# Performance work log

Measured on AMD Instinct MI355X. Metric: run time of the kernel, lower is better.

Reference implementation:

```python
import jax, jax.numpy as jnp
import numpy as np

N, E = 10000, 320000
NF, HF = 256, 256  # input_nf/output_nf, hidden_nf
EPS = 1e-8


def setup_inputs() -> dict:
    key = jax.random.key(0)
    ks = jax.random.split(key, 20)
    h = jax.random.normal(ks[0], (N, NF), jnp.float32)
    coord = jax.random.normal(ks[1], (N, 3), jnp.float32)
    edge_index = jax.random.randint(ks[2], (2, E), 0, N, jnp.int32)

    def dense(k, fan_in, fan_out, scale=None):
        s = scale if scale is not None else 1.0 / np.sqrt(fan_in)
        W = jax.random.normal(k, (fan_in, fan_out), jnp.float32) * s
        b = jnp.zeros((fan_out,), jnp.float32)
        return W, b

    We1, be1 = dense(ks[3], 2 * NF + 1, HF)   # edge_mlp layer 1
    We2, be2 = dense(ks[4], HF, HF)           # edge_mlp layer 2
    Wn1, bn1 = dense(ks[5], HF + NF, HF)      # node_mlp layer 1
    Wn2, bn2 = dense(ks[6], HF, NF)           # node_mlp layer 2
    Wc1, bc1 = dense(ks[7], HF, HF)           # coord_mlp layer 1
    Wc2, bc2 = dense(ks[8], HF, 1, scale=0.001)  # coord_mlp final, tiny init (xavier gain=0.001)
    return dict(h=h, coord=coord, edge_index=edge_index,
                We1=We1, be1=be1, We2=We2, be2=be2,
                Wn1=Wn1, bn1=bn1, Wn2=Wn2, bn2=bn2,
                Wc1=Wc1, bc1=bc1, Wc2=Wc2, bc2=bc2)


def _segment_sum(data, seg_ids, num_segments):
    return jax.ops.segment_sum(data, seg_ids, num_segments=num_segments)


def reference(h, coord, edge_index, We1, be1, We2, be2, Wn1, bn1, Wn2, bn2, Wc1, bc1, Wc2, bc2):
    row, col = edge_index[0], edge_index[1]

    # coord2radial
    coord_diff = coord[row] - coord[col]                    # [E, 3]
    radial = jnp.sum(coord_diff ** 2, axis=1, keepdims=True)  # [E, 1]

    # edge model: MLP on [h_i, h_j, ||x_i - x_j||^2]
    edge_in = jnp.concatenate([h[row], h[col], radial], axis=1)  # [E, 2*NF+1]
    e = jax.nn.silu(edge_in @ We1 + be1)
    edge_feat = jax.nn.silu(e @ We2 + be2)                  # [E, HF]

    # coord model: coord_diff * coord_mlp(edge_feat), mean-aggregated
    c = jax.nn.silu(edge_feat @ Wc1 + bc1)
    trans = coord_diff * (c @ Wc2 + bc2)                    # [E, 3]
    agg_c = _segment_sum(trans, row, coord.shape[0])
    count = _segment_sum(jnp.ones_like(trans), row, coord.shape[0])
    coord_out = coord + agg_c / jnp.clip(count, 1.0)

    # node model: sum-aggregate edge features, concat with h, MLP
    agg_h = _segment_sum(edge_feat, row, h.shape[0])        # [N, HF]
    node_in = jnp.concatenate([h, agg_h], axis=1)           # [N, HF+NF]
    n = jax.nn.silu(node_in @ Wn1 + bn1)
    h_out = n @ Wn2 + bn2                                   # [N, NF]

    return h_out, coord_out
```

## Files before the change

kernel.cpp:

```cpp
#include <hip/hip_runtime.h>
#include <hip/hip_bf16.h>

typedef __bf16 bf16;
typedef __attribute__((ext_vector_type(8))) __bf16 bf16x8;
typedef __attribute__((ext_vector_type(4))) float f32x4;

static_assert(sizeof(bf16x8) == 16, "bf16x8 must be 16B");

constexpr int N_NODES = 10000;
constexpr int N_EDGES = 320000;
constexpr int KPAD    = 264;

__device__ __forceinline__ float silu_f(float x) { return x / (1.0f + __expf(-x)); }

__device__ __forceinline__ unsigned pk_bf16(float lo, float hi) {
  unsigned a = __float_as_uint(lo) + 0x8000u;
  unsigned b = __float_as_uint(hi) + 0x8000u;
  return __builtin_amdgcn_perm(b, a, 0x07060302u);
}

__device__ __forceinline__ void mfmaT_k256(const bf16* __restrict__ WT, int wstride, int koff,
                                           const bf16* Albs, int w, int r, int q, f32x4 acc[4][4]) {
  for (int k0 = 0; k0 < 256; k0 += 32) {
    bf16x8 a[4], b[4];
#pragma unroll
    for (int mi = 0; mi < 4; ++mi)
      a[mi] = *(const bf16x8*)(WT + (size_t)(w * 64 + 16 * mi + r) * wstride + koff + k0 + q * 8);
#pragma unroll
    for (int ni = 0; ni < 4; ++ni)
      b[ni] = *(const bf16x8*)(Albs + (16 * ni + r) * KPAD + k0 + q * 8);
#pragma unroll
    for (int mi = 0; mi < 4; ++mi)
#pragma unroll
      for (int ni = 0; ni < 4; ++ni)
        acc[mi][ni] = __builtin_amdgcn_mfma_f32_16x16x32_bf16(a[mi], b[ni], acc[mi][ni], 0, 0, 0);
  }
}

__global__ __launch_bounds__(256) void prep_kernel(
    const float* __restrict__ h, const float* __restrict__ We1, const float* __restrict__ We2,
    const float* __restrict__ Wn1, const float* __restrict__ Wn2, const float* __restrict__ Wc1,
    const int* __restrict__ eidx,
    bf16* __restrict__ Hb, bf16* __restrict__ We1T, bf16* __restrict__ Wn1T,
    bf16* __restrict__ We2T, bf16* __restrict__ Wn2T, bf16* __restrict__ Wc1T,
    int* __restrict__ hist) {
  int bid = blockIdx.x, tid = threadIdx.x;
  if (bid < 10000) { int i = bid * 256 + tid; Hb[i] = (bf16)h[i]; return; }
  if (bid >= 11792) {
    int e = (bid - 11792) * 256 + tid;
    if (e < N_EDGES) atomicAdd(&hist[eidx[e]], 1);
    return;
  }
  int t = (bid - 10000) * 256 + tid;
  if (t < 131072) { int k = t >> 8, j = t & 255; We1T[j * 512 + k] = (bf16)We1[k * 256 + j]; return; }
  t -= 131072;
  if (t < 131072) { int k = t >> 8, j = t & 255; Wn1T[j * 512 + k] = (bf16)Wn1[k * 256 + j]; return; }
  t -= 131072;
  if (t < 65536) { int k = t >> 8, j = t & 255; We2T[j * 256 + k] = (bf16)We2[k * 256 + j]; return; }
  t -= 65536;
  if (t < 65536) { int k = t >> 8, j = t & 255; Wn2T[j * 256 + k] = (bf16)Wn2[k * 256 + j]; return; }
  t -= 65536;
  if (t < 65536) { int k = t >> 8, j = t & 255; Wc1T[j * 256 + k] = (bf16)Wc1[k * 256 + j]; return; }
}

__global__ __launch_bounds__(256) void scan_kernel(const int* __restrict__ hist,
                                                   int* __restrict__ base, int* __restrict__ cursor) {
  __shared__ int partial[256];
  int t = threadIdx.x;
  int s = 0;
  for (int i = 0; i < 40; ++i) { int idx = t * 40 + i; if (idx < N_NODES) s += hist[idx]; }
  partial[t] = s;
  __syncthreads();
  for (int d = 1; d < 256; d <<= 1) {
    int v = (t >= d) ? partial[t - d] : 0;
    __syncthreads();
    partial[t] += v;
    __syncthreads();
  }
  int run = partial[t] - s;
  for (int i = 0; i < 40; ++i) {
    int idx = t * 40 + i;
    if (idx < N_NODES) { base[idx] = run; cursor[idx] = run; run += hist[idx]; }
  }
}

__global__ __launch_bounds__(256) void scatter_kernel(const int* __restrict__ eidx, int* __restrict__ cursor,
                                                      int* __restrict__ rs, int* __restrict__ cs) {
  int e = blockIdx.x * 256 + threadIdx.x;
  if (e < N_EDGES) {
    int r = eidx[e], c = eidx[N_EDGES + e];
    int p = atomicAdd(&cursor[r], 1);
    rs[p] = r; cs[p] = c;
  }
}

__global__ __launch_bounds__(256, 2) void gemm_pq(const bf16* __restrict__ Hb,
                                                  const bf16* __restrict__ We1T,
                                                  const float* __restrict__ be1,
                                                  bf16* __restrict__ P, bf16* __restrict__ Q) {
  int tid = threadIdx.x, w = tid >> 6, lane = tid & 63, r = lane & 15, q = lane >> 4;
  int m0 = blockIdx.x * 64;
  int koff = blockIdx.y ? 256 : 0;
  bf16* OUT = blockIdx.y ? Q : P;
  bool addb = (blockIdx.y == 0);
  f32x4 acc[4][4];
#pragma unroll
  for (int mi = 0; mi < 4; ++mi)
#pragma unroll
    for (int ni = 0; ni < 4; ++ni) acc[mi][ni] = (f32x4){0.f, 0.f, 0.f, 0.f};

  for (int k0 = 0; k0 < 256; k0 += 32) {
    bf16x8 a[4], b[4];
#pragma unroll
    for (int mi = 0; mi < 4; ++mi)
      a[mi] = *(const bf16x8*)(We1T + (size_t)(w * 64 + 16 * mi + r) * 512 + koff + k0 + q * 8);
#pragma unroll
    for (int ni = 0; ni < 4; ++ni) {
      int m = m0 + 16 * ni + r; if (m > N_NODES - 1) m = N_NODES - 1;
      b[ni] = *(const bf16x8*)(Hb + (size_t)m * 256 + k0 + q * 8);
    }
#pragma unroll
    for (int mi = 0; mi < 4; ++mi)
#pragma unroll
      for (int ni = 0; ni < 4; ++ni)
        acc[mi][ni] = __builtin_amdgcn_mfma_f32_16x16x32_bf16(a[mi], b[ni], acc[mi][ni], 0, 0, 0);
  }
#pragma unroll
  for (int mi = 0; mi < 4; ++mi) {
    int ch = w * 64 + 16 * mi + 4 * q;
    float4 bv = addb ? *(const float4*)(be1 + ch) : (float4){0.f, 0.f, 0.f, 0.f};
#pragma unroll
    for (int ni = 0; ni < 4; ++ni) {
      int m = m0 + 16 * ni + r;
      if (m < N_NODES) {
        uint2 o;
        o.x = pk_bf16(acc[mi][ni][0] + bv.x, acc[mi][ni][1] + bv.y);
        o.y = pk_bf16(acc[mi][ni][2] + bv.z, acc[mi][ni][3] + bv.w);
        *(uint2*)(OUT + (size_t)m * 256 + ch) = o;
      }
    }
  }
}

__global__ __launch_bounds__(256, 4) void edge_kernel(
    const float* __restrict__ coord, const int* __restrict__ rs, const int* __restrict__ cs,
    const float* __restrict__ We1,
    const float* __restrict__ be2, const float* __restrict__ bc1,
    const float* __restrict__ Wc2, const float* __restrict__ bc2,
    const bf16* __restrict__ P, const bf16* __restrict__ Q,
    const bf16* __restrict__ We2T, const bf16* __restrict__ Wc1T,
    float* __restrict__ agg_h, float* __restrict__ agg_c) {
  __shared__ __align__(16) bf16 buf[64 * KPAD];
  __shared__ int s_row[64], s_col[64];
  __shared__ float s_rad[64], s_cd[64][3], s_part[64][4], s_scal[64];
  __shared__ int s_rs[65];
  __shared__ int s_nrun;

  int tid = threadIdx.x;
  int e0 = blockIdx.x * 64;
  int w = tid >> 6, lane = tid & 63, r = lane & 15, q = lane >> 4;

  if (tid < 64) {
    int e = e0 + tid;
    int ri = rs[e], ci = cs[e];
    s_row[tid] = ri; s_col[tid] = ci;
    float dx = coord[3 * ri + 0] - coord[3 * ci + 0];
    float dy = coord[3 * ri + 1] - coord[3 * ci + 1];
    float dz = coord[3 * ri + 2] - coord[3 * ci + 2];
    s_cd[tid][0] = dx; s_cd[tid][1] = dy; s_cd[tid][2] = dz;
    s_rad[tid] = dx * dx + dy * dy + dz * dz;
  }
  __syncthreads();

  if (tid < 64) {
    bool bnd = (tid == 0) || (s_row[tid] != s_row[tid - 1]);
    unsigned long long m = __ballot(bnd);
    int rank = __popcll(m & ((1ull << tid) - 1ull));
    if (bnd) s_rs[rank] = tid;
    if (tid == 0) { int R = __popcll(m); s_nrun = R; s_rs[R] = 64; }
  }

  {
    int off = (tid & 31) * 8;
    int esub = tid >> 5;
    float4 wa = *(const float4*)(We1 + 512 * 256 + off);
    float4 wb = *(const float4*)(We1 + 512 * 256 + off + 4);
#pragma unroll
    for (int p = 0; p < 8; ++p) {
      int e = p * 8 + esub;
      int ri = s_row[e], ci = s_col[e];
      bf16x8 pv = *(const bf16x8*)(P + (size_t)ri * 256 + off);
      bf16x8 qv = *(const bf16x8*)(Q + (size_t)ci * 256 + off);
      float rad = s_rad[e];
      float f0 = silu_f((float)pv[0] + (float)qv[0] + rad * wa.x);
      float f1 = silu_f((float)pv[1] + (float)qv[1] + rad * wa.y);
      float f2 = silu_f((float)pv[2] + (float)qv[2] + rad * wa.z);
      float f3 = silu_f((float)pv[3] + (float)qv[3] + rad * wa.w);
      float f4 = silu_f((float)pv[4] + (float)qv[4] + rad * wb.x);
      float f5 = silu_f((float)pv[5] + (float)qv[5] + rad * wb.y);
      float f6 = silu_f((float)pv[6] + (float)qv[6] + rad * wb.z);
      float f7 = silu_f((float)pv[7] + (float)qv[7] + rad * wb.w);
      uint4 o;
      o.x = pk_bf16(f0, f1); o.y = pk_bf16(f2, f3);
      o.z = pk_bf16(f4, f5); o.w = pk_bf16(f6, f7);
      *(uint4*)(buf + e * KPAD + off) = o;
    }
  }
  __syncthreads();

  {
    f32x4 acc[4][4];
#pragma unroll
    for (int mi = 0; mi < 4; ++mi)
#pragma unroll
      for (int ni = 0; ni < 4; ++ni) acc[mi][ni] = (f32x4){0.f, 0.f, 0.f, 0.f};
    mfmaT_k256(We2T, 256, 0, buf, w, r, q, acc);
    __syncthreads();
#pragma unroll
    for (int mi = 0; mi < 4; ++mi) {
      int ch = w * 64 + 16 * mi + 4 * q;
      float4 bv = *(const float4*)(be2 + ch);
#pragma unroll
      for (int ni = 0; ni < 4; ++ni) {
        int edge = 16 * ni + r;
        float f0 = silu_f(acc[mi][ni][0] + bv.x);
        float f1 = silu_f(acc[mi][ni][1] + bv.y);
        float f2 = silu_f(acc[mi][ni][2] + bv.z);
        float f3 = silu_f(acc[mi][ni][3] + bv.w);
        uint2 o; o.x = pk_bf16(f0, f1); o.y = pk_bf16(f2, f3);
        *(uint2*)(buf + edge * KPAD + ch) = o;
      }
    }
  }
  __syncthreads();

  f32x4 acc2[4][4];
#pragma unroll
  for (int mi = 0; mi < 4; ++mi)
#pragma unroll
    for (int ni = 0; ni < 4; ++ni) acc2[mi][ni] = (f32x4){0.f, 0.f, 0.f, 0.f};
  mfmaT_k256(Wc1T, 256, 0, buf, w, r, q, acc2);

  {
    int R = s_nrun;
    for (int rr = 0; rr < R; ++rr) {
      int st = s_rs[rr], en = s_rs[rr + 1];
      float s = 0.f;
      for (int e = st; e < en; ++e) s += (float)buf[e * KPAD + tid];
      atomicAdd(&agg_h[(size_t)s_row[st] * 256 + tid], s);
    }
  }
  __syncthreads();

#pragma unroll
  for (int mi = 0; mi < 4; ++mi) {
    int ch = w * 64 + 16 * mi + 4 * q;
    float4 bv = *(const float4*)(bc1 + ch);
#pragma unroll
    for (int ni = 0; ni < 4; ++ni) {
      int edge = 16 * ni + r;
      float f0 = silu_f(acc2[mi][ni][0] + bv.x);
      float f1 = silu_f(acc2[mi][ni][1] + bv.y);
      float f2 = silu_f(acc2[mi][ni][2] + bv.z);
      float f3 = silu_f(acc2[mi][ni][3] + bv.w);
      uint2 o; o.x = pk_bf16(f0, f1); o.y = pk_bf16(f2, f3);
      *(uint2*)(buf + edge * KPAD + ch) = o;
    }
  }
  __syncthreads();

  {
    int e = tid >> 2, p = tid & 3;
    float s = 0.f;
#pragma unroll
    for (int kk = 0; kk < 64; kk += 8) {
      bf16x8 v = *(const bf16x8*)(buf + e * KPAD + p * 64 + kk);
      float4 w0 = *(const float4*)(Wc2 + p * 64 + kk);
      float4 w1 = *(const float4*)(Wc2 + p * 64 + kk + 4);
      s += (float)v[0] * w0.x + (float)v[1] * w0.y + (float)v[2] * w0.z + (float)v[3] * w0.w
         + (float)v[4] * w1.x + (float)v[5] * w1.y + (float)v[6] * w1.z + (float)v[7] * w1.w;
    }
    s_part[e][p] = s;
  }
  __syncthreads();
  if (tid < 64)
    s_scal[tid] = s_part[tid][0] + s_part[tid][1] + s_part[tid][2] + s_part[tid][3] + bc2[0];
  __syncthreads();

  if (tid < 3) {
    int R = s_nrun;
    for (int rr = 0; rr < R; ++rr) {
      int st = s_rs[rr], en = s_rs[rr + 1];
      float s = 0.f;
      for (int e = st; e < en; ++e) s += s_cd[e][tid] * s_scal[e];
      atomicAdd(&agg_c[3 * s_row[st] + tid], s);
    }
  }
}

__global__ __launch_bounds__(256, 2) void node_kernel(
    const bf16* __restrict__ Hb, const float* __restrict__ agg_h,
    const int* __restrict__ hist, const float* __restrict__ coord, const float* __restrict__ agg_c,
    const bf16* __restrict__ Wn1T, const bf16* __restrict__ Wn2T,
    const float* __restrict__ bn1, const float* __restrict__ bn2,
    float* __restrict__ h_out, float* __restrict__ coord_out) {
  __shared__ __align__(16) bf16 buf[64 * KPAD];
  int tid = threadIdx.x, w = tid >> 6, lane = tid & 63, r = lane & 15, q = lane >> 4;
  int m0 = blockIdx.x * 64;

  if (tid < 64) {
    int m = m0 + tid;
    if (m < N_NODES) {
      float c = (float)hist[m]; if (c < 1.f) c = 1.f;
      coord_out[3 * m + 0] = coord[3 * m + 0] + agg_c[3 * m + 0] / c;
      coord_out[3 * m + 1] = coord[3 * m + 1] + agg_c[3 * m + 1] / c;
      coord_out[3 * m + 2] = coord[3 * m + 2] + agg_c[3 * m + 2] / c;
    }
  }

  f32x4 acc[4][4];
#pragma unroll
  for (int mi = 0; mi < 4; ++mi)
#pragma unroll
    for (int ni = 0; ni < 4; ++ni) acc[mi][ni] = (f32x4){0.f, 0.f, 0.f, 0.f};
  for (int k0 = 0; k0 < 256; k0 += 32) {
    bf16x8 a[4], b[4];
#pragma unroll
    for (int mi = 0; mi < 4; ++mi)
      a[mi] = *(const bf16x8*)(Wn1T + (size_t)(w * 64 + 16 * mi + r) * 512 + k0 + q * 8);
#pragma unroll
    for (int ni = 0; ni < 4; ++ni) {
      int m = m0 + 16 * ni + r; if (m > N_NODES - 1) m = N_NODES - 1;
      b[ni] = *(const bf16x8*)(Hb + (size_t)m * 256 + k0 + q * 8);
    }
#pragma unroll
    for (int mi = 0; mi < 4; ++mi)
#pragma unroll
      for (int ni = 0; ni < 4; ++ni)
        acc[mi][ni] = __builtin_amdgcn_mfma_f32_16x16x32_bf16(a[mi], b[ni], acc[mi][ni], 0, 0, 0);
  }
  for (int k0 = 0; k0 < 256; k0 += 32) {
    bf16x8 a[4], b[4];
#pragma unroll
    for (int mi = 0; mi < 4; ++mi)
      a[mi] = *(const bf16x8*)(Wn1T + (size_t)(w * 64 + 16 * mi + r) * 512 + 256 + k0 + q * 8);
#pragma unroll
    for (int ni = 0; ni < 4; ++ni) {
      int m = m0 + 16 * ni + r; if (m > N_NODES - 1) m = N_NODES - 1;
      const float* ap = agg_h + (size_t)m * 256 + k0 + q * 8;
      float4 u = *(const float4*)ap;
      float4 v = *(const float4*)(ap + 4);
      uint4 o;
      o.x = pk_bf16(u.x, u.y); o.y = pk_bf16(u.z, u.w);
      o.z = pk_bf16(v.x, v.y); o.w = pk_bf16(v.z, v.w);
      b[ni] = *(const bf16x8*)&o;
    }
#pragma unroll
    for (int mi = 0; mi < 4; ++mi)
#pragma unroll
      for (int ni = 0; ni < 4; ++ni)
        acc[mi][ni] = __builtin_amdgcn_mfma_f32_16x16x32_bf16(a[mi], b[ni], acc[mi][ni], 0, 0, 0);
  }
  __syncthreads();
#pragma unroll
  for (int mi = 0; mi < 4; ++mi) {
    int ch = w * 64 + 16 * mi + 4 * q;
    float4 bv = *(const float4*)(bn1 + ch);
#pragma unroll
    for (int ni = 0; ni < 4; ++ni) {
      int lm = 16 * ni + r;
      float f0 = silu_f(acc[mi][ni][0] + bv.x);
      float f1 = silu_f(acc[mi][ni][1] + bv.y);
      float f2 = silu_f(acc[mi][ni][2] + bv.z);
      float f3 = silu_f(acc[mi][ni][3] + bv.w);
      uint2 o; o.x = pk_bf16(f0, f1); o.y = pk_bf16(f2, f3);
      *(uint2*)(buf + lm * KPAD + ch) = o;
    }
  }
  __syncthreads();
  f32x4 acc2[4][4];
#pragma unroll
  for (int mi = 0; mi < 4; ++mi)
#pragma unroll
    for (int ni = 0; ni < 4; ++ni) acc2[mi][ni] = (f32x4){0.f, 0.f, 0.f, 0.f};
  mfmaT_k256(Wn2T, 256, 0, buf, w, r, q, acc2);
#pragma unroll
  for (int mi = 0; mi < 4; ++mi) {
    int ch = w * 64 + 16 * mi + 4 * q;
    float4 bv = *(const float4*)(bn2 + ch);
#pragma unroll
    for (int ni = 0; ni < 4; ++ni) {
      int m = m0 + 16 * ni + r;
      if (m < N_NODES) {
        float4 o;
        o.x = acc2[mi][ni][0] + bv.x;
        o.y = acc2[mi][ni][1] + bv.y;
        o.z = acc2[mi][ni][2] + bv.z;
        o.w = acc2[mi][ni][3] + bv.w;
        *(float4*)(h_out + (size_t)m * 256 + ch) = o;
      }
    }
  }
}

extern "C" void kernel_launch(void* const* d_in, const int* in_sizes, int n_in,
                              void* d_out, int out_size, void* d_ws, size_t ws_size,
                              hipStream_t stream) {
  const float* h     = (const float*)d_in[0];
  const float* coord = (const float*)d_in[1];
  const int*   eidx  = (const int*)d_in[2];
  const float* We1 = (const float*)d_in[3];
  const float* be1 = (const float*)d_in[4];
  const float* We2 = (const float*)d_in[5];
  const float* be2 = (const float*)d_in[6];
  const float* Wn1 = (const float*)d_in[7];
  const float* bn1 = (const float*)d_in[8];
  const float* Wn2 = (const float*)d_in[9];
  const float* bn2 = (const float*)d_in[10];
  const float* Wc1 = (const float*)d_in[11];
  const float* bc1 = (const float*)d_in[12];
  const float* Wc2 = (const float*)d_in[13];
  const float* bc2 = (const float*)d_in[14];

  char* ws = (char*)d_ws;
  float* agg_h = (float*)(ws + 0);
  float* agg_c = (float*)(ws + 10240000);
  int*   hist  = (int*)  (ws + 10360000);
  int*   base  = (int*)  (ws + 10400000);
  int*   cursor= (int*)  (ws + 10440000);
  int*   rs    = (int*)  (ws + 10480000);
  int*   cs    = (int*)  (ws + 11760000);
  bf16* Hb   = (bf16*)(ws + 13040000);
  bf16* P    = (bf16*)(ws + 18160000);
  bf16* Q    = (bf16*)(ws + 23280000);
  bf16* We1T = (bf16*)(ws + 28400000);
  bf16* Wn1T = (bf16*)(ws + 28662144);
  bf16* We2T = (bf16*)(ws + 28924288);
  bf16* Wn2T = (bf16*)(ws + 29055360);
  bf16* Wc1T = (bf16*)(ws + 29186432);

  float* h_out = (float*)d_out;
  float* coord_out = h_out + (size_t)N_NODES * 256;

  hipMemsetAsync(ws, 0, 10400000, stream);
  prep_kernel<<<13042, 256, 0, stream>>>(h, We1, We2, Wn1, Wn2, Wc1, eidx,
                                         Hb, We1T, Wn1T, We2T, Wn2T, Wc1T, hist);
  scan_kernel<<<1, 256, 0, stream>>>(hist, base, cursor);
  scatter_kernel<<<1250, 256, 0, stream>>>(eidx, cursor, rs, cs);
  gemm_pq<<<dim3(157, 2), 256, 0, stream>>>(Hb, We1T, be1, P, Q);
  edge_kernel<<<5000, 256, 0, stream>>>(coord, rs, cs, We1, be2, bc1, Wc2, bc2,
                                        P, Q, We2T, Wc1T, agg_h, agg_c);
  node_kernel<<<157, 256, 0, stream>>>(Hb, agg_h, hist, coord, agg_c,
                                       Wn1T, Wn2T, bn1, bn2, h_out, coord_out);
}
```

Baseline: 458.2 us.

## Double edge and node kernel waves to 8, fuse coord head into register epilogue

Edge and node kernels now launch 512 threads (8 waves), and each wave computes 32 output channels instead of 64, halving per-wave accumulators to raise occupancy. The Wc2 dot product is computed straight from the Wc1 accumulators in registers and reduced through shared atomics, removing a shared-memory write-back pass and two barriers. SiLU and the coord mean use hardware reciprocal instead of division. The risks are extra shared-atomic contention, more barrier participants, and slightly lower reciprocal precision.

```diff
diff --git a/kernel.cpp b/kernel.cpp
--- a/kernel.cpp
+++ b/kernel.cpp
@@ -11,7 +11,9 @@
 constexpr int N_EDGES = 320000;
 constexpr int KPAD    = 264;
 
-__device__ __forceinline__ float silu_f(float x) { return x / (1.0f + __expf(-x)); }
+__device__ __forceinline__ float silu_f(float x) {
+  return x * __builtin_amdgcn_rcpf(1.0f + __expf(-x));
+}
 
 __device__ __forceinline__ unsigned pk_bf16(float lo, float hi) {
   unsigned a = __float_as_uint(lo) + 0x8000u;
@@ -19,18 +21,18 @@
   return __builtin_amdgcn_perm(b, a, 0x07060302u);
 }
 
-__device__ __forceinline__ void mfmaT_k256(const bf16* __restrict__ WT, int wstride, int koff,
-                                           const bf16* Albs, int w, int r, int q, f32x4 acc[4][4]) {
+__device__ __forceinline__ void mfmaT2_k256(const bf16* __restrict__ WT, int wstride,
+                                            const bf16* Albs, int r, int q, f32x4 acc[2][4]) {
   for (int k0 = 0; k0 < 256; k0 += 32) {
-    bf16x8 a[4], b[4];
-#pragma unroll
-    for (int mi = 0; mi < 4; ++mi)
-      a[mi] = *(const bf16x8*)(WT + (size_t)(w * 64 + 16 * mi + r) * wstride + koff + k0 + q * 8);
+    bf16x8 a[2], b[4];
+#pragma unroll
+    for (int mi = 0; mi < 2; ++mi)
+      a[mi] = *(const bf16x8*)(WT + (size_t)(16 * mi + r) * wstride + k0 + q * 8);
 #pragma unroll
     for (int ni = 0; ni < 4; ++ni)
       b[ni] = *(const bf16x8*)(Albs + (16 * ni + r) * KPAD + k0 + q * 8);
 #pragma unroll
-    for (int mi = 0; mi < 4; ++mi)
+    for (int mi = 0; mi < 2; ++mi)
 #pragma unroll
       for (int ni = 0; ni < 4; ++ni)
         acc[mi][ni] = __builtin_amdgcn_mfma_f32_16x16x32_bf16(a[mi], b[ni], acc[mi][ni], 0, 0, 0);
@@ -142,7 +144,7 @@
   }
 }
 
-__global__ __launch_bounds__(256, 4) void edge_kernel(
+__global__ __launch_bounds__(512, 6) void edge_kernel(
     const float* __restrict__ coord, const int* __restrict__ rs, const int* __restrict__ cs,
     const float* __restrict__ We1,
     const float* __restrict__ be2, const float* __restrict__ bc1,
@@ -152,7 +154,7 @@
     float* __restrict__ agg_h, float* __restrict__ agg_c) {
   __shared__ __align__(16) bf16 buf[64 * KPAD];
   __shared__ int s_row[64], s_col[64];
-  __shared__ float s_rad[64], s_cd[64][3], s_part[64][4], s_scal[64];
+  __shared__ float s_rad[64], s_cd[64][3], s_scal[64];
   __shared__ int s_rs[65];
   __shared__ int s_nrun;
 
@@ -169,6 +171,7 @@
     float dz = coord[3 * ri + 2] - coord[3 * ci + 2];
     s_cd[tid][0] = dx; s_cd[tid][1] = dy; s_cd[tid][2] = dz;
     s_rad[tid] = dx * dx + dy * dy + dz * dz;
+    s_scal[tid] = 0.f;
   }
   __syncthreads();
 
@@ -186,8 +189,8 @@
     float4 wa = *(const float4*)(We1 + 512 * 256 + off);
     float4 wb = *(const float4*)(We1 + 512 * 256 + off + 4);
 #pragma unroll
-    for (int p = 0; p < 8; ++p) {
-      int e = p * 8 + esub;
+    for (int p = 0; p < 4; ++p) {
+      int e = p * 16 + esub;
       int ri = s_row[e], ci = s_col[e];
       bf16x8 pv = *(const bf16x8*)(P + (size_t)ri * 256 + off);
       bf16x8 qv = *(const bf16x8*)(Q + (size_t)ci * 256 + off);
@@ -209,16 +212,16 @@
   __syncthreads();
 
   {
-    f32x4 acc[4][4];
-#pragma unroll
-    for (int mi = 0; mi < 4; ++mi)
+    f32x4 acc[2][4];
+#pragma unroll
+    for (int mi = 0; mi < 2; ++mi)
 #pragma unroll
       for (int ni = 0; ni < 4; ++ni) acc[mi][ni] = (f32x4){0.f, 0.f, 0.f, 0.f};
-    mfmaT_k256(We2T, 256, 0, buf, w, r, q, acc);
+    mfmaT2_k256(We2T + (size_t)(w * 32) * 256, 256, buf, r, q, acc);
     __syncthreads();
 #pragma unroll
-    for (int mi = 0; mi < 4; ++mi) {
-      int ch = w * 64 + 16 * mi + 4 * q;
+    for (int mi = 0; mi < 2; ++mi) {
+      int ch = w * 32 + 16 * mi + 4 * q;
       float4 bv = *(const float4*)(be2 + ch);
 #pragma unroll
       for (int ni = 0; ni < 4; ++ni) {
@@ -234,57 +237,44 @@
   }
   __syncthreads();
 
-  f32x4 acc2[4][4];
-#pragma unroll
-  for (int mi = 0; mi < 4; ++mi)
+  f32x4 acc2[2][4];
+#pragma unroll
+  for (int mi = 0; mi < 2; ++mi)
 #pragma unroll
     for (int ni = 0; ni < 4; ++ni) acc2[mi][ni] = (f32x4){0.f, 0.f, 0.f, 0.f};
-  mfmaT_k256(Wc1T, 256, 0, buf, w, r, q, acc2);
+  mfmaT2_k256(Wc1T + (size_t)(w * 32) * 256, 256, buf, r, q, acc2);
 
   {
+    int col = tid & 255, start = tid >> 8;
     int R = s_nrun;
-    for (int rr = 0; rr < R; ++rr) {
+    for (int rr = start; rr < R; rr += 2) {
       int st = s_rs[rr], en = s_rs[rr + 1];
       float s = 0.f;
-      for (int e = st; e < en; ++e) s += (float)buf[e * KPAD + tid];
-      atomicAdd(&agg_h[(size_t)s_row[st] * 256 + tid], s);
-    }
-  }
-  __syncthreads();
-
-#pragma unroll
-  for (int mi = 0; mi < 4; ++mi) {
-    int ch = w * 64 + 16 * mi + 4 * q;
-    float4 bv = *(const float4*)(bc1 + ch);
-#pragma unroll
-    for (int ni = 0; ni < 4; ++ni) {
-      int edge = 16 * ni + r;
-      float f0 = silu_f(acc2[mi][ni][0] + bv.x);
-      float f1 = silu_f(acc2[mi][ni][1] + bv.y);
-      float f2 = silu_f(acc2[mi][ni][2] + bv.z);
-      float f3 = silu_f(acc2[mi][ni][3] + bv.w);
-      uint2 o; o.x = pk_bf16(f0, f1); o.y = pk_bf16(f2, f3);
-      *(uint2*)(buf + edge * KPAD + ch) = o;
-    }
-  }
-  __syncthreads();
+      for (int e = st; e < en; ++e) s += (float)buf[e * KPAD + col];
+      atomicAdd(&agg_h[(size_t)s_row[st] * 256 + col], s);
+    }
+  }
 
   {
-    int e = tid >> 2, p = tid & 3;
-    float s = 0.f;
-#pragma unroll
-    for (int kk = 0; kk < 64; kk += 8) {
-      bf16x8 v = *(const bf16x8*)(buf + e * KPAD + p * 64 + kk);
-      float4 w0 = *(const float4*)(Wc2 + p * 64 + kk);
-      float4 w1 = *(const float4*)(Wc2 + p * 64 + kk + 4);
-      s += (float)v[0] * w0.x + (float)v[1] * w0.y + (float)v[2] * w0.z + (float)v[3] * w0.w
-         + (float)v[4] * w1.x + (float)v[5] * w1.y + (float)v[6] * w1.z + (float)v[7] * w1.w;
-    }
-    s_part[e][p] = s;
-  }
-  __syncthreads();
-  if (tid < 64)
-    s_scal[tid] = s_part[tid][0] + s_part[tid][1] + s_part[tid][2] + s_part[tid][3] + bc2[0];
+    float part[4] = {0.f, 0.f, 0.f, 0.f};
+#pragma unroll
+    for (int mi = 0; mi < 2; ++mi) {
+      int ch = w * 32 + 16 * mi + 4 * q;
+      float4 bv = *(const float4*)(bc1 + ch);
+      float4 wv = *(const float4*)(Wc2 + ch);
+#pragma unroll
+      for (int ni = 0; ni < 4; ++ni) {
+        float f0 = silu_f(acc2[mi][ni][0] + bv.x);
+        float f1 = silu_f(acc2[mi][ni][1] + bv.y);
+        float f2 = silu_f(acc2[mi][ni][2] + bv.z);
+        float f3 = silu_f(acc2[mi][ni][3] + bv.w);
+        part[ni] += f0 * wv.x + f1 * wv.y + f2 * wv.z + f3 * wv.w;
+      }
+    }
+#pragma unroll
+    for (int ni = 0; ni < 4; ++ni)
+      atomicAdd(&s_scal[16 * ni + r], part[ni]);
+  }
   __syncthreads();
 
   if (tid < 3) {
@@ -292,13 +282,13 @@
     for (int rr = 0; rr < R; ++rr) {
       int st = s_rs[rr], en = s_rs[rr + 1];
       float s = 0.f;
-      for (int e = st; e < en; ++e) s += s_cd[e][tid] * s_scal[e];
+      for (int e = st; e < en; ++e) s += s_cd[e][tid] * (s_scal[e] + bc2[0]);
       atomicAdd(&agg_c[3 * s_row[st] + tid], s);
     }
   }
 }
 
-__global__ __launch_bounds__(256, 2) void node_kernel(
+__global__ __launch_bounds__(512, 6) void node_kernel(
     const bf16* __restrict__ Hb, const float* __restrict__ agg_h,
     const int* __restrict__ hist, const float* __restrict__ coord, const float* __restrict__ agg_c,
     const bf16* __restrict__ Wn1T, const bf16* __restrict__ Wn2T,
@@ -312,38 +302,40 @@
     int m = m0 + tid;
     if (m < N_NODES) {
       float c = (float)hist[m]; if (c < 1.f) c = 1.f;
-      coord_out[3 * m + 0] = coord[3 * m + 0] + agg_c[3 * m + 0] / c;
-      coord_out[3 * m + 1] = coord[3 * m + 1] + agg_c[3 * m + 1] / c;
-      coord_out[3 * m + 2] = coord[3 * m + 2] + agg_c[3 * m + 2] / c;
-    }
-  }
-
-  f32x4 acc[4][4];
-#pragma unroll
-  for (int mi = 0; mi < 4; ++mi)
+      float inv = __builtin_amdgcn_rcpf(c);
+      coord_out[3 * m + 0] = coord[3 * m + 0] + agg_c[3 * m + 0] * inv;
+      coord_out[3 * m + 1] = coord[3 * m + 1] + agg_c[3 * m + 1] * inv;
+      coord_out[3 * m + 2] = coord[3 * m + 2] + agg_c[3 * m + 2] * inv;
+    }
+  }
+
+  f32x4 acc[2][4];
+#pragma unroll
+  for (int mi = 0; mi < 2; ++mi)
 #pragma unroll
     for (int ni = 0; ni < 4; ++ni) acc[mi][ni] = (f32x4){0.f, 0.f, 0.f, 0.f};
+  const bf16* BT1 = Wn1T + (size_t)(w * 32) * 512;
   for (int k0 = 0; k0 < 256; k0 += 32) {
-    bf16x8 a[4], b[4];
-#pragma unroll
-    for (int mi = 0; mi < 4; ++mi)
-      a[mi] = *(const bf16x8*)(Wn1T + (size_t)(w * 64 + 16 * mi + r) * 512 + k0 + q * 8);
+    bf16x8 a[2], b[4];
+#pragma unroll
+    for (int mi = 0; mi < 2; ++mi)
+      a[mi] = *(const bf16x8*)(BT1 + (size_t)(16 * mi + r) * 512 + k0 + q * 8);
 #pragma unroll
     for (int ni = 0; ni < 4; ++ni) {
       int m = m0 + 16 * ni + r; if (m > N_NODES - 1) m = N_NODES - 1;
       b[ni] = *(const bf16x8*)(Hb + (size_t)m * 256 + k0 + q * 8);
     }
 #pragma unroll
-    for (int mi = 0; mi < 4; ++mi)
+    for (int mi = 0; mi < 2; ++mi)
 #pragma unroll
       for (int ni = 0; ni < 4; ++ni)
         acc[mi][ni] = __builtin_amdgcn_mfma_f32_16x16x32_bf16(a[mi], b[ni], acc[mi][ni], 0, 0, 0);
   }
   for (int k0 = 0; k0 < 256; k0 += 32) {
-    bf16x8 a[4], b[4];
-#pragma unroll
-    for (int mi = 0; mi < 4; ++mi)
-      a[mi] = *(const bf16x8*)(Wn1T + (size_t)(w * 64 + 16 * mi + r) * 512 + 256 + k0 + q * 8);
+    bf16x8 a[2], b[4];
+#pragma unroll
+    for (int mi = 0; mi < 2; ++mi)
+      a[mi] = *(const bf16x8*)(BT1 + (size_t)(16 * mi + r) * 512 + 256 + k0 + q * 8);
 #pragma unroll
     for (int ni = 0; ni < 4; ++ni) {
       int m = m0 + 16 * ni + r; if (m > N_NODES - 1) m = N_NODES - 1;
@@ -356,15 +348,15 @@
       b[ni] = *(const bf16x8*)&o;
     }
 #pragma unroll
-    for (int mi = 0; mi < 4; ++mi)
+    for (int mi = 0; mi < 2; ++mi)
 #pragma unroll
       for (int ni = 0; ni < 4; ++ni)
         acc[mi][ni] = __builtin_amdgcn_mfma_f32_16x16x32_bf16(a[mi], b[ni], acc[mi][ni], 0, 0, 0);
   }
   __syncthreads();
 #pragma unroll
-  for (int mi = 0; mi < 4; ++mi) {
-    int ch = w * 64 + 16 * mi + 4 * q;
+  for (int mi = 0; mi < 2; ++mi) {
+    int ch = w * 32 + 16 * mi + 4 * q;
     float4 bv = *(const float4*)(bn1 + ch);
 #pragma unroll
     for (int ni = 0; ni < 4; ++ni) {
@@ -378,15 +370,15 @@
     }
   }
   __syncthreads();
-  f32x4 acc2[4][4];
-#pragma unroll
-  for (int mi = 0; mi < 4; ++mi)
+  f32x4 acc2[2][4];
+#pragma unroll
+  for (int mi = 0; mi < 2; ++mi)
 #pragma unroll
     for (int ni = 0; ni < 4; ++ni) acc2[mi][ni] = (f32x4){0.f, 0.f, 0.f, 0.f};
-  mfmaT_k256(Wn2T, 256, 0, buf, w, r, q, acc2);
-#pragma unroll
-  for (int mi = 0; mi < 4; ++mi) {
-    int ch = w * 64 + 16 * mi + 4 * q;
+  mfmaT2_k256(Wn2T + (size_t)(w * 32) * 256, 256, buf, r, q, acc2);
+#pragma unroll
+  for (int mi = 0; mi < 2; ++mi) {
+    int ch = w * 32 + 16 * mi + 4 * q;
     float4 bv = *(const float4*)(bn2 + ch);
 #pragma unroll
     for (int ni = 0; ni < 4; ++ni) {
@@ -448,8 +440,8 @@
   scan_kernel<<<1, 256, 0, stream>>>(hist, base, cursor);
   scatter_kernel<<<1250, 256, 0, stream>>>(eidx, cursor, rs, cs);
   gemm_pq<<<dim3(157, 2), 256, 0, stream>>>(Hb, We1T, be1, P, Q);
-  edge_kernel<<<5000, 256, 0, stream>>>(coord, rs, cs, We1, be2, bc1, Wc2, bc2,
+  edge_kernel<<<5000, 512, 0, stream>>>(coord, rs, cs, We1, be2, bc1, Wc2, bc2,
                                         P, Q, We2T, Wc1T, agg_h, agg_c);
-  node_kernel<<<157, 256, 0, stream>>>(Hb, agg_h, hist, coord, agg_c,
+  node_kernel<<<157, 512, 0, stream>>>(Hb, agg_h, hist, coord, agg_c,
                                        Wn1T, Wn2T, bn1, bn2, h_out, coord_out);
 }
```

After: 482.8 us. 1.05x slower.

## Process four edge tiles per block and fuse coord MLP output in registers

Applied to the files above, without the earlier changes.

The edge kernel now handles 256 edges per block, looping over four 64-edge tiles. Row and column indices, radial and coord_diff are loaded once up front, and segment boundaries are precomputed as per-tile ballot masks, so each column's segmented reduction becomes a single pass. The final Wc2 dot product is done in registers straight from the MFMA accumulators and combined with shared-memory atomics, which removes a shared-memory round trip and several barriers. Smaller changes: vectorised h-to-bf16 conversion in prep, rcp-based SiLU and division, and the edge kernel's occupancy hint lowered from 4 to 3 blocks. The cost is fewer blocks, a different register and occupancy balance, and a serial 64-step reduction loop per column.

```diff
diff --git a/kernel.cpp b/kernel.cpp
--- a/kernel.cpp
+++ b/kernel.cpp
@@ -10,8 +10,11 @@
 constexpr int N_NODES = 10000;
 constexpr int N_EDGES = 320000;
 constexpr int KPAD    = 264;
-
-__device__ __forceinline__ float silu_f(float x) { return x / (1.0f + __expf(-x)); }
+constexpr int NT      = 4;
+
+__device__ __forceinline__ float silu_f(float x) {
+  return x * __builtin_amdgcn_rcpf(1.0f + __expf(-x));
+}
 
 __device__ __forceinline__ unsigned pk_bf16(float lo, float hi) {
   unsigned a = __float_as_uint(lo) + 0x8000u;
@@ -19,13 +22,13 @@
   return __builtin_amdgcn_perm(b, a, 0x07060302u);
 }
 
-__device__ __forceinline__ void mfmaT_k256(const bf16* __restrict__ WT, int wstride, int koff,
+__device__ __forceinline__ void mfmaT_k256(const bf16* __restrict__ WT, int wstride,
                                            const bf16* Albs, int w, int r, int q, f32x4 acc[4][4]) {
   for (int k0 = 0; k0 < 256; k0 += 32) {
     bf16x8 a[4], b[4];
 #pragma unroll
     for (int mi = 0; mi < 4; ++mi)
-      a[mi] = *(const bf16x8*)(WT + (size_t)(w * 64 + 16 * mi + r) * wstride + koff + k0 + q * 8);
+      a[mi] = *(const bf16x8*)(WT + (size_t)(w * 64 + 16 * mi + r) * wstride + k0 + q * 8);
 #pragma unroll
     for (int ni = 0; ni < 4; ++ni)
       b[ni] = *(const bf16x8*)(Albs + (16 * ni + r) * KPAD + k0 + q * 8);
@@ -45,13 +48,19 @@
     bf16* __restrict__ We2T, bf16* __restrict__ Wn2T, bf16* __restrict__ Wc1T,
     int* __restrict__ hist) {
   int bid = blockIdx.x, tid = threadIdx.x;
-  if (bid < 10000) { int i = bid * 256 + tid; Hb[i] = (bf16)h[i]; return; }
-  if (bid >= 11792) {
-    int e = (bid - 11792) * 256 + tid;
+  if (bid < 2500) {
+    int i = (bid * 256 + tid) * 4;
+    float4 v = *(const float4*)(h + i);
+    uint2 o; o.x = pk_bf16(v.x, v.y); o.y = pk_bf16(v.z, v.w);
+    *(uint2*)(Hb + i) = o;
+    return;
+  }
+  if (bid >= 4292) {
+    int e = (bid - 4292) * 256 + tid;
     if (e < N_EDGES) atomicAdd(&hist[eidx[e]], 1);
     return;
   }
-  int t = (bid - 10000) * 256 + tid;
+  int t = (bid - 2500) * 256 + tid;
   if (t < 131072) { int k = t >> 8, j = t & 255; We1T[j * 512 + k] = (bf16)We1[k * 256 + j]; return; }
   t -= 131072;
   if (t < 131072) { int k = t >> 8, j = t & 255; Wn1T[j * 512 + k] = (bf16)Wn1[k * 256 + j]; return; }
@@ -142,7 +151,7 @@
   }
 }
 
-__global__ __launch_bounds__(256, 4) void edge_kernel(
+__global__ __launch_bounds__(256, 3) void edge_kernel(
     const float* __restrict__ coord, const int* __restrict__ rs, const int* __restrict__ cs,
     const float* __restrict__ We1,
     const float* __restrict__ be2, const float* __restrict__ bc1,
@@ -151,16 +160,18 @@
     const bf16* __restrict__ We2T, const bf16* __restrict__ Wc1T,
     float* __restrict__ agg_h, float* __restrict__ agg_c) {
   __shared__ __align__(16) bf16 buf[64 * KPAD];
-  __shared__ int s_row[64], s_col[64];
-  __shared__ float s_rad[64], s_cd[64][3], s_part[64][4], s_scal[64];
-  __shared__ int s_rs[65];
-  __shared__ int s_nrun;
+  __shared__ int s_row[256], s_col[256];
+  __shared__ float s_rad[256], s_cd[256][3];
+  __shared__ float s_scal[64];
+  __shared__ unsigned long long s_bmask[NT];
 
   int tid = threadIdx.x;
-  int e0 = blockIdx.x * 64;
+  int e0 = blockIdx.x * 256;
   int w = tid >> 6, lane = tid & 63, r = lane & 15, q = lane >> 4;
-
-  if (tid < 64) {
+  int off = (tid & 31) * 8;
+  int esub = tid >> 5;
+
+  {
     int e = e0 + tid;
     int ri = rs[e], ci = cs[e];
     s_row[tid] = ri; s_col[tid] = ci;
@@ -171,26 +182,27 @@
     s_rad[tid] = dx * dx + dy * dy + dz * dz;
   }
   __syncthreads();
-
-  if (tid < 64) {
-    bool bnd = (tid == 0) || (s_row[tid] != s_row[tid - 1]);
-    unsigned long long m = __ballot(bnd);
-    int rank = __popcll(m & ((1ull << tid) - 1ull));
-    if (bnd) s_rs[rank] = tid;
-    if (tid == 0) { int R = __popcll(m); s_nrun = R; s_rs[R] = 64; }
-  }
-
   {
-    int off = (tid & 31) * 8;
-    int esub = tid >> 5;
-    float4 wa = *(const float4*)(We1 + 512 * 256 + off);
-    float4 wb = *(const float4*)(We1 + 512 * 256 + off + 4);
+    int e = w * 64 + lane;
+    bool bnd = (lane < 63) && (s_row[e] != s_row[e + 1]);
+    unsigned long long m = __ballot(bnd) | (1ull << 63);
+    if (lane == 0) s_bmask[w] = m;
+  }
+
+  float4 wa = *(const float4*)(We1 + 512 * 256 + off);
+  float4 wb = *(const float4*)(We1 + 512 * 256 + off + 4);
+  float bc2v = bc2[0];
+
+  for (int t = 0; t < NT; ++t) {
+    int eb = t * 64;
+
+    if (tid < 64) s_scal[tid] = 0.f;
 #pragma unroll
     for (int p = 0; p < 8; ++p) {
-      int e = p * 8 + esub;
-      int ri = s_row[e], ci = s_col[e];
-      bf16x8 pv = *(const bf16x8*)(P + (size_t)ri * 256 + off);
-      bf16x8 qv = *(const bf16x8*)(Q + (size_t)ci * 256 + off);
+      int el = p * 8 + esub;
+      int e = eb + el;
+      bf16x8 pv = *(const bf16x8*)(P + (size_t)s_row[e] * 256 + off);
+      bf16x8 qv = *(const bf16x8*)(Q + (size_t)s_col[e] * 256 + off);
       float rad = s_rad[e];
       float f0 = silu_f((float)pv[0] + (float)qv[0] + rad * wa.x);
       float f1 = silu_f((float)pv[1] + (float)qv[1] + rad * wa.y);
@@ -203,19 +215,18 @@
       uint4 o;
       o.x = pk_bf16(f0, f1); o.y = pk_bf16(f2, f3);
       o.z = pk_bf16(f4, f5); o.w = pk_bf16(f6, f7);
-      *(uint4*)(buf + e * KPAD + off) = o;
-    }
-  }
-  __syncthreads();
-
-  {
+      *(uint4*)(buf + el * KPAD + off) = o;
+    }
+    __syncthreads();
+
     f32x4 acc[4][4];
 #pragma unroll
     for (int mi = 0; mi < 4; ++mi)
 #pragma unroll
       for (int ni = 0; ni < 4; ++ni) acc[mi][ni] = (f32x4){0.f, 0.f, 0.f, 0.f};
-    mfmaT_k256(We2T, 256, 0, buf, w, r, q, acc);
-    __syncthreads();
+    mfmaT_k256(We2T, 256, buf, w, r, q, acc);
+    __syncthreads();
+
 #pragma unroll
     for (int mi = 0; mi < 4; ++mi) {
       int ch = w * 64 + 16 * mi + 4 * q;
@@ -231,70 +242,63 @@
         *(uint2*)(buf + edge * KPAD + ch) = o;
       }
     }
-  }
-  __syncthreads();
-
-  f32x4 acc2[4][4];
-#pragma unroll
-  for (int mi = 0; mi < 4; ++mi)
-#pragma unroll
-    for (int ni = 0; ni < 4; ++ni) acc2[mi][ni] = (f32x4){0.f, 0.f, 0.f, 0.f};
-  mfmaT_k256(Wc1T, 256, 0, buf, w, r, q, acc2);
-
-  {
-    int R = s_nrun;
-    for (int rr = 0; rr < R; ++rr) {
-      int st = s_rs[rr], en = s_rs[rr + 1];
+    __syncthreads();
+
+    f32x4 acc2[4][4];
+#pragma unroll
+    for (int mi = 0; mi < 4; ++mi)
+#pragma unroll
+      for (int ni = 0; ni < 4; ++ni) acc2[mi][ni] = (f32x4){0.f, 0.f, 0.f, 0.f};
+    mfmaT_k256(Wc1T, 256, buf, w, r, q, acc2);
+
+    {
+      unsigned long long bm = s_bmask[t];
       float s = 0.f;
-      for (int e = st; e < en; ++e) s += (float)buf[e * KPAD + tid];
-      atomicAdd(&agg_h[(size_t)s_row[st] * 256 + tid], s);
-    }
-  }
-  __syncthreads();
-
-#pragma unroll
-  for (int mi = 0; mi < 4; ++mi) {
-    int ch = w * 64 + 16 * mi + 4 * q;
-    float4 bv = *(const float4*)(bc1 + ch);
-#pragma unroll
-    for (int ni = 0; ni < 4; ++ni) {
-      int edge = 16 * ni + r;
-      float f0 = silu_f(acc2[mi][ni][0] + bv.x);
-      float f1 = silu_f(acc2[mi][ni][1] + bv.y);
-      float f2 = silu_f(acc2[mi][ni][2] + bv.z);
-      float f3 = silu_f(acc2[mi][ni][3] + bv.w);
-      uint2 o; o.x = pk_bf16(f0, f1); o.y = pk_bf16(f2, f3);
-      *(uint2*)(buf + edge * KPAD + ch) = o;
-    }
-  }
-  __syncthreads();
-
-  {
-    int e = tid >> 2, p = tid & 3;
-    float s = 0.f;
-#pragma unroll
-    for (int kk = 0; kk < 64; kk += 8) {
-      bf16x8 v = *(const bf16x8*)(buf + e * KPAD + p * 64 + kk);
-      float4 w0 = *(const float4*)(Wc2 + p * 64 + kk);
-      float4 w1 = *(const float4*)(Wc2 + p * 64 + kk + 4);
-      s += (float)v[0] * w0.x + (float)v[1] * w0.y + (float)v[2] * w0.z + (float)v[3] * w0.w
-         + (float)v[4] * w1.x + (float)v[5] * w1.y + (float)v[6] * w1.z + (float)v[7] * w1.w;
-    }
-    s_part[e][p] = s;
-  }
-  __syncthreads();
-  if (tid < 64)
-    s_scal[tid] = s_part[tid][0] + s_part[tid][1] + s_part[tid][2] + s_part[tid][3] + bc2[0];
-  __syncthreads();
-
-  if (tid < 3) {
-    int R = s_nrun;
-    for (int rr = 0; rr < R; ++rr) {
-      int st = s_rs[rr], en = s_rs[rr + 1];
+#pragma unroll 4
+      for (int e = 0; e < 64; ++e) {
+        s += (float)buf[e * KPAD + tid];
+        if ((bm >> e) & 1ull) {
+          atomicAdd(&agg_h[(size_t)s_row[eb + e] * 256 + tid], s);
+          s = 0.f;
+        }
+      }
+    }
+
+    {
+      float part[4] = {0.f, 0.f, 0.f, 0.f};
+#pragma unroll
+      for (int mi = 0; mi < 4; ++mi) {
+        int ch = w * 64 + 16 * mi + 4 * q;
+        float4 bv = *(const float4*)(bc1 + ch);
+        float4 wv = *(const float4*)(Wc2 + ch);
+#pragma unroll
+        for (int ni = 0; ni < 4; ++ni) {
+          float f0 = silu_f(acc2[mi][ni][0] + bv.x);
+          float f1 = silu_f(acc2[mi][ni][1] + bv.y);
+          float f2 = silu_f(acc2[mi][ni][2] + bv.z);
+          float f3 = silu_f(acc2[mi][ni][3] + bv.w);
+          part[ni] += f0 * wv.x + f1 * wv.y + f2 * wv.z + f3 * wv.w;
+        }
+      }
+#pragma unroll
+      for (int ni = 0; ni < 4; ++ni)
+        atomicAdd(&s_scal[16 * ni + r], part[ni]);
+    }
+    __syncthreads();
+
+    if (tid < 3) {
+      unsigned long long bm = s_bmask[t];
       float s = 0.f;
-      for (int e = st; e < en; ++e) s += s_cd[e][tid] * s_scal[e];
-      atomicAdd(&agg_c[3 * s_row[st] + tid], s);
-    }
+#pragma unroll 8
+      for (int e = 0; e < 64; ++e) {
+        s += s_cd[eb + e][tid] * (s_scal[e] + bc2v);
+        if ((bm >> e) & 1ull) {
+          atomicAdd(&agg_c[3 * s_row[eb + e] + tid], s);
+          s = 0.f;
+        }
+      }
+    }
+    __syncthreads();
   }
 }
 
@@ -312,9 +316,10 @@
     int m = m0 + tid;
     if (m < N_NODES) {
       float c = (float)hist[m]; if (c < 1.f) c = 1.f;
-      coord_out[3 * m + 0] = coord[3 * m + 0] + agg_c[3 * m + 0] / c;
-      coord_out[3 * m + 1] = coord[3 * m + 1] + agg_c[3 * m + 1] / c;
-      coord_out[3 * m + 2] = coord[3 * m + 2] + agg_c[3 * m + 2] / c;
+      float inv = __builtin_amdgcn_rcpf(c);
+      coord_out[3 * m + 0] = coord[3 * m + 0] + agg_c[3 * m + 0] * inv;
+      coord_out[3 * m + 1] = coord[3 * m + 1] + agg_c[3 * m + 1] * inv;
+      coord_out[3 * m + 2] = coord[3 * m + 2] + agg_c[3 * m + 2] * inv;
     }
   }
 
@@ -383,7 +388,7 @@
   for (int mi = 0; mi < 4; ++mi)
 #pragma unroll
     for (int ni = 0; ni < 4; ++ni) acc2[mi][ni] = (f32x4){0.f, 0.f, 0.f, 0.f};
-  mfmaT_k256(Wn2T, 256, 0, buf, w, r, q, acc2);
+  mfmaT_k256(Wn2T, 256, buf, w, r, q, acc2);
 #pragma unroll
   for (int mi = 0; mi < 4; ++mi) {
     int ch = w * 64 + 16 * mi + 4 * q;
@@ -443,12 +448,12 @@
   float* coord_out = h_out + (size_t)N_NODES * 256;
 
   hipMemsetAsync(ws, 0, 10400000, stream);
-  prep_kernel<<<13042, 256, 0, stream>>>(h, We1, We2, Wn1, Wn2, Wc1, eidx,
-                                         Hb, We1T, Wn1T, We2T, Wn2T, Wc1T, hist);
+  prep_kernel<<<5542, 256, 0, stream>>>(h, We1, We2, Wn1, Wn2, Wc1, eidx,
+                                        Hb, We1T, Wn1T, We2T, Wn2T, Wc1T, hist);
   scan_kernel<<<1, 256, 0, stream>>>(hist, base, cursor);
   scatter_kernel<<<1250, 256, 0, stream>>>(eidx, cursor, rs, cs);
   gemm_pq<<<dim3(157, 2), 256, 0, stream>>>(Hb, We1T, be1, P, Q);
-  edge_kernel<<<5000, 256, 0, stream>>>(coord, rs, cs, We1, be2, bc1, Wc2, bc2,
+  edge_kernel<<<1250, 256, 0, stream>>>(coord, rs, cs, We1, be2, bc1, Wc2, bc2,
                                         P, Q, We2T, Wc1T, agg_h, agg_c);
   node_kernel<<<157, 256, 0, stream>>>(Hb, agg_h, hist, coord, agg_c,
                                        Wn1T, Wn2T, bn1, bn2, h_out, coord_out);
```

New measurement: 644.0 us. 40.5% more time.
